# Performance work log

Measured on AMD Instinct MI355X. Metric: run time of the kernel, lower is better.

Reference implementation:

```python
import jax, jax.numpy as jnp
import numpy as np

TAU = 0.4
EPS = 1e-8


def setup_inputs() -> dict:
    key = jax.random.key(0)
    k1, k2 = jax.random.split(key)
    B, N, C, M = 4, 4096, 256, 2048
    l_feat = jax.random.normal(k1, (B, N, C), dtype=jnp.float32)
    g_feat = jax.random.normal(k2, (B, C, M), dtype=jnp.float32)
    return {"l_feat": l_feat, "g_feat": g_feat}


def reference(l_feat, g_feat):
    # l_feat: [B, N, C], g_feat: [B, C, M]
    # cosine similarity over channel dim C (torch CosineSimilarity, dim=2)
    l_norm = jnp.linalg.norm(l_feat, axis=2)          # [B, N]
    g_norm = jnp.linalg.norm(g_feat, axis=1)          # [B, M]
    dot = jnp.einsum('bnc,bcm->bnm', l_feat, g_feat)  # [B, N, M]
    cos_sim = dot / jnp.maximum(l_norm[:, :, None] * g_norm[:, None, :], EPS)
    sim = jnp.exp(cos_sim / TAU)                      # [B, N, M]
    # diag_embed(rowsum) followed by linalg.inv and bmm is exactly
    # row-wise division by the degree (row sum)
    sim = sim / jnp.sum(sim, axis=2, keepdims=True)
    # bmm(sim, g_feat^T): [B,N,M] x [B,M,C] -> [B,N,C]
    g_enh = jnp.einsum('bnm,bcm->bnc', sim, g_feat)
    return l_feat + g_enh
```

## Files before the change

### kernel.cpp

```cpp
#include <hip/hip_runtime.h>

#define B_ 4
#define N_ 4096
#define C_ 256
#define M_ 2048

typedef __attribute__((ext_vector_type(8))) short short8;
typedef __attribute__((ext_vector_type(4))) short short4v;
typedef __attribute__((ext_vector_type(4))) float f32x4;

union U16x8 { uint4 u4; unsigned short us[8]; short8 s8; };
union U16x4 { uint2 u2; unsigned short us[4]; short4v s4; };

__device__ __forceinline__ float bf2f(unsigned short h) {
    unsigned int u = ((unsigned int)h) << 16;
    return __builtin_bit_cast(float, u);
}
__device__ __forceinline__ unsigned short f2bf(float f) {
    unsigned int u = __builtin_bit_cast(unsigned int, f);
    u += 0x7FFFu + ((u >> 16) & 1u);
    return (unsigned short)(u >> 16);
}

#define GLB_AS(p) ((const __attribute__((address_space(1))) unsigned int*)(p))
#define LDS_AS(p) ((__attribute__((address_space(3))) unsigned int*)(p))

__device__ __forceinline__ f32x4 mfma16x16(short4v a, short4v b, f32x4 c) {
#if __has_builtin(__builtin_amdgcn_mfma_f32_16x16x16bf16_1k)
    return __builtin_amdgcn_mfma_f32_16x16x16bf16_1k(a, b, c, 0, 0, 0);
#else
    asm("v_mfma_f32_16x16x16_bf16 %0, %1, %2, %0" : "+v"(c) : "v"(a), "v"(b));
    return c;
#endif
}

__global__ __launch_bounds__(256) void k_norm(const float* __restrict__ g,
                                              float* __restrict__ invgn) {
    __shared__ float red[4][64];
    const int b = blockIdx.y, m0 = blockIdx.x * 64;
    const int tid = threadIdx.x;
    const int ml = tid & 63, cq = tid >> 6;
    const float* gb = g + (size_t)b * C_ * M_ + m0 + ml;
    float ss = 0.f;
#pragma unroll 8
    for (int i = 0; i < 64; ++i) {
        float v = gb[(size_t)(cq * 64 + i) * M_];
        ss += v * v;
    }
    red[cq][ml] = ss;
    __syncthreads();
    if (cq == 0) {
        float t = red[0][ml] + red[1][ml] + red[2][ml] + red[3][ml];
        invgn[b * M_ + m0 + ml] = 1.f / fmaxf(sqrtf(t), 1e-8f);
    }
}

__global__ __launch_bounds__(256) void k_cast(const float* __restrict__ g,
                                              const float* __restrict__ invgn,
                                              unsigned short* __restrict__ gcm,
                                              unsigned short* __restrict__ gmc) {
    __shared__ unsigned short T[64 * 66];
    __shared__ float sInv[64];
    const int b = blockIdx.z, c0 = blockIdx.y * 64, m0 = blockIdx.x * 64;
    const int tid = threadIdx.x;
    if (tid < 64) sInv[tid] = invgn[b * M_ + m0 + tid];
    __syncthreads();
    const float* gbase = g + ((size_t)b * C_ + c0) * M_ + m0;
    unsigned short* gcmb = gcm + ((size_t)b * C_ + c0) * M_ + m0;
#pragma unroll
    for (int j = 0; j < 4; ++j) {
        int id = tid + 256 * j;
        int ci = id >> 4, mq = (id & 15) * 4;
        float4 v = *(const float4*)(gbase + (size_t)ci * M_ + mq);
        uint2 pk;
        pk.x = (unsigned)f2bf(v.x) | ((unsigned)f2bf(v.y) << 16);
        pk.y = (unsigned)f2bf(v.z) | ((unsigned)f2bf(v.w) << 16);
        *(uint2*)(gcmb + (size_t)ci * M_ + mq) = pk;
        T[ci * 66 + mq + 0] = f2bf(v.x * sInv[mq + 0]);
        T[ci * 66 + mq + 1] = f2bf(v.y * sInv[mq + 1]);
        T[ci * 66 + mq + 2] = f2bf(v.z * sInv[mq + 2]);
        T[ci * 66 + mq + 3] = f2bf(v.w * sInv[mq + 3]);
    }
    __syncthreads();
    unsigned short* gmcb = gmc + ((size_t)b * M_ + m0) * C_ + c0;
#pragma unroll
    for (int j = 0; j < 2; ++j) {
        int id = tid + 256 * j;
        int mr = id >> 3, cc8 = (id & 7) * 8;
        U16x8 t;
#pragma unroll
        for (int k = 0; k < 8; ++k) t.us[k] = T[(cc8 + k) * 66 + mr];
        *(uint4*)(gmcb + (size_t)mr * C_ + cc8) = t.u4;
    }
}

__global__ __launch_bounds__(256, 2) void k_main(
    const float* __restrict__ l,
    const unsigned short* __restrict__ gcm,
    const unsigned short* __restrict__ gmc,
    float* __restrict__ out)
{
    __shared__ __align__(16) char sMem[66048];
    unsigned short* sGmc = (unsigned short*)sMem;
    unsigned short* sGcm = (unsigned short*)(sMem + 32768);
    float (*sDenW)[32] = (float (*)[32])(sMem + 65536);

    const int tid = threadIdx.x;
    const int w = tid >> 6;
    const int lane = tid & 63;
    const int l15 = lane & 15;
    const int quad = lane >> 4;

    const int bid = blockIdx.x;
    const int xcd = bid & 7;
    const int b = xcd >> 1;
    const int row0 = (((bid >> 3) << 1) | (xcd & 1)) * 32;

    int goffA[8], goffB[8];
#pragma unroll
    for (int i = 0; i < 8; ++i) {
        int p = (w * 8 + i) * 64 + lane;
        int rA = p >> 5;
        goffA[i] = rA * 256 + (((p & 31) ^ (rA & 31)) << 3);
        int rB = p >> 3;
        goffB[i] = rB * 2048 + (((p & 7) ^ ((rB >> 1) & 7)) << 3);
    }

    const unsigned short* gmc_b = gmc + (size_t)b * M_ * C_;
    const unsigned short* gcm_b = gcm + (size_t)b * C_ * M_;

    auto dmaA = [&](int m0) {
#pragma unroll
        for (int i = 0; i < 8; ++i)
            __builtin_amdgcn_global_load_lds(GLB_AS(gmc_b + (size_t)m0 * 256 + goffA[i]),
                                             LDS_AS(&sGmc[(w * 8 + i) * 512]), 16, 0, 0);
    };
    auto dmaB = [&](int m0) {
#pragma unroll
        for (int i = 0; i < 8; ++i)
            __builtin_amdgcn_global_load_lds(GLB_AS(gcm_b + (size_t)m0 + goffB[i]),
                                             LDS_AS(&sGcm[(w * 8 + i) * 512]), 16, 0, 0);
    };

    dmaA(0);
    dmaB(0);

    short8 qf[2][8];
#pragma unroll
    for (int rt = 0; rt < 2; ++rt) {
        const float* lrow = l + ((size_t)b * N_ + row0 + rt * 16 + l15) * C_;
        U16x8 qt[8];
        float ss = 0.f;
#pragma unroll
        for (int kk = 0; kk < 8; ++kk) {
            float4 x0 = *(const float4*)(lrow + kk * 32 + quad * 8);
            float4 x1 = *(const float4*)(lrow + kk * 32 + quad * 8 + 4);
            ss += x0.x*x0.x + x0.y*x0.y + x0.z*x0.z + x0.w*x0.w;
            ss += x1.x*x1.x + x1.y*x1.y + x1.z*x1.z + x1.w*x1.w;
            qt[kk].us[0] = f2bf(x0.x); qt[kk].us[1] = f2bf(x0.y);
            qt[kk].us[2] = f2bf(x0.z); qt[kk].us[3] = f2bf(x0.w);
            qt[kk].us[4] = f2bf(x1.x); qt[kk].us[5] = f2bf(x1.y);
            qt[kk].us[6] = f2bf(x1.z); qt[kk].us[7] = f2bf(x1.w);
        }
        ss += __shfl_xor(ss, 16);
        ss += __shfl_xor(ss, 32);
        const float invl = 1.0f / fmaxf(sqrtf(ss), 1e-8f);
#pragma unroll
        for (int kk = 0; kk < 8; ++kk) {
            U16x8 t;
#pragma unroll
            for (int j = 0; j < 8; ++j) t.us[j] = f2bf(bf2f(qt[kk].us[j]) * invl);
            qf[rt][kk] = t.s8;
        }
    }

    __syncthreads();

    f32x4 zero = {0.f, 0.f, 0.f, 0.f};
    f32x4 o[2][16];
#pragma unroll
    for (int i = 0; i < 2; ++i)
#pragma unroll
        for (int j = 0; j < 16; ++j) o[i][j] = zero;
    float dl0 = 0.f, dl1 = 0.f;

    const unsigned short* gAbase = &sGmc[(w * 16 + l15) * 256];
    const int rxor = (w * 16 + l15) & 31;
    const int chunkXor = (w * 4 + quad) ^ (l15 & 14);
    const unsigned short* gBbase = &sGcm[l15 * 64 + (chunkXor << 2)];

    for (int mt = 0; mt < 32; ++mt) {
        f32x4 sa0 = zero, sa1 = zero;
#pragma unroll
        for (int kk = 0; kk < 8; ++kk) {
            short8 ag = *(const short8*)&gAbase[((kk * 4 + quad) ^ rxor) << 3];
            sa0 = __builtin_amdgcn_mfma_f32_16x16x32_bf16(ag, qf[0][kk], sa0, 0, 0, 0);
            sa1 = __builtin_amdgcn_mfma_f32_16x16x32_bf16(ag, qf[1][kk], sa1, 0, 0, 0);
        }
        U16x4 pk0, pk1;
#pragma unroll
        for (int r = 0; r < 4; ++r) {
            float p0 = exp2f(sa0[r] * 3.6067376022224085f);
            float p1 = exp2f(sa1[r] * 3.6067376022224085f);
            dl0 += p0; dl1 += p1;
            pk0.us[r] = f2bf(p0);
            pk1.us[r] = f2bf(p1);
        }
        __syncthreads();
        if (mt < 31) dmaA((mt + 1) * 64);

#pragma unroll
        for (int ct = 0; ct < 16; ++ct) {
            short4v bb = *(const short4v*)&gBbase[ct * 1024];
            o[0][ct] = mfma16x16(pk0.s4, bb, o[0][ct]);
            o[1][ct] = mfma16x16(pk1.s4, bb, o[1][ct]);
        }
        __syncthreads();
        if (mt < 31) dmaB((mt + 1) * 64);
    }

    {
        float d0 = dl0;
        d0 += __shfl_xor(d0, 16);
        d0 += __shfl_xor(d0, 32);
        float d1 = dl1;
        d1 += __shfl_xor(d1, 16);
        d1 += __shfl_xor(d1, 32);
        if (quad == 0) {
            sDenW[w][l15] = d0;
            sDenW[w][16 + l15] = d1;
        }
    }

    f32x4* red = (f32x4*)sMem;
    const int wbase = w * 1024 + quad * 16 + l15;
    const int rbase0 = (4 * w) * 64 + quad * 16 + l15;
    f32x4 oacc0[4], oacc1[4];

    __syncthreads();
#pragma unroll
    for (int j = 0; j < 16; ++j) red[wbase + j * 64] = o[0][j];
    __syncthreads();
#pragma unroll
    for (int jj = 0; jj < 4; ++jj) {
        const int base = rbase0 + jj * 64;
        oacc0[jj] = red[base] + red[base + 1024] + red[base + 2048] + red[base + 3072];
    }
    __syncthreads();
#pragma unroll
    for (int j = 0; j < 16; ++j) red[wbase + j * 64] = o[1][j];
    __syncthreads();
#pragma unroll
    for (int jj = 0; jj < 4; ++jj) {
        const int base = rbase0 + jj * 64;
        oacc1[jj] = red[base] + red[base + 1024] + red[base + 2048] + red[base + 3072];
    }

    const float* lb = l + ((size_t)b * N_ + row0) * C_;
    float* ob = out + ((size_t)b * N_ + row0) * C_;
#pragma unroll
    for (int r = 0; r < 4; ++r) {
        {
            const int row = quad * 4 + r;
            const float inv = 1.f / (sDenW[0][row] + sDenW[1][row] + sDenW[2][row] + sDenW[3][row]);
            const size_t rb = (size_t)row * C_;
#pragma unroll
            for (int jj = 0; jj < 4; ++jj) {
                const int c = w * 64 + jj * 16 + l15;
                ob[rb + c] = lb[rb + c] + oacc0[jj][r] * inv;
            }
        }
        {
            const int row = 16 + quad * 4 + r;
            const float inv = 1.f / (sDenW[0][row] + sDenW[1][row] + sDenW[2][row] + sDenW[3][row]);
            const size_t rb = (size_t)row * C_;
#pragma unroll
            for (int jj = 0; jj < 4; ++jj) {
                const int c = w * 64 + jj * 16 + l15;
                ob[rb + c] = lb[rb + c] + oacc1[jj][r] * inv;
            }
        }
    }
}

extern "C" void kernel_launch(void* const* d_in, const int* in_sizes, int n_in,
                              void* d_out, int out_size, void* d_ws, size_t ws_size,
                              hipStream_t stream) {
    (void)in_sizes; (void)n_in; (void)out_size; (void)ws_size;
    const float* l = (const float*)d_in[0];
    const float* g = (const float*)d_in[1];
    float* outp = (float*)d_out;

    char* ws = (char*)d_ws;
    unsigned short* gmc = (unsigned short*)ws;
    unsigned short* gcm = (unsigned short*)(ws + (size_t)B_ * M_ * C_ * 2);
    float* invgn = (float*)(ws + 2 * (size_t)B_ * M_ * C_ * 2);

    k_norm<<<dim3(M_ / 64, B_), 256, 0, stream>>>(g, invgn);
    k_cast<<<dim3(M_ / 64, C_ / 64, B_), 256, 0, stream>>>(g, invgn, gcm, gmc);
    k_main<<<dim3(N_ / 32 * B_), 256, 0, stream>>>(l, gcm, gmc, outp);
}
```

Measured before the change: 144.9 us.

## Fuse norm and cast prep kernels; double rows per main block with 512 threads

The g-norm and bf16 cast/transpose kernels are merged into one prep kernel that computes the inverse norms in shared memory and then loops over channel tiles, removing one launch and the invgn round trip. The main kernel now uses 512 threads covering 64 query rows (two row-halves of 4 waves each) sharing the same staged g tiles in LDS. This halves the global/LDS traffic for g per row processed and halves the grid size. In exchange, the prep kernel has less parallelism (128 blocks looping serially over C), and the cross-wave reduction is serialized into four rounds.

```diff
diff --git a/kernel.cpp b/kernel.cpp
--- a/kernel.cpp
+++ b/kernel.cpp
@@ -34,12 +34,16 @@
 #endif
 }
 
-__global__ __launch_bounds__(256) void k_norm(const float* __restrict__ g,
-                                              float* __restrict__ invgn) {
+__global__ __launch_bounds__(256) void k_prep(const float* __restrict__ g,
+                                              unsigned short* __restrict__ gcm,
+                                              unsigned short* __restrict__ gmc) {
     __shared__ float red[4][64];
+    __shared__ float sInv[64];
+    __shared__ unsigned short T[64 * 66];
     const int b = blockIdx.y, m0 = blockIdx.x * 64;
     const int tid = threadIdx.x;
     const int ml = tid & 63, cq = tid >> 6;
+
     const float* gb = g + (size_t)b * C_ * M_ + m0 + ml;
     float ss = 0.f;
 #pragma unroll 8
@@ -51,75 +55,70 @@
     __syncthreads();
     if (cq == 0) {
         float t = red[0][ml] + red[1][ml] + red[2][ml] + red[3][ml];
-        invgn[b * M_ + m0 + ml] = 1.f / fmaxf(sqrtf(t), 1e-8f);
-    }
-}
-
-__global__ __launch_bounds__(256) void k_cast(const float* __restrict__ g,
-                                              const float* __restrict__ invgn,
-                                              unsigned short* __restrict__ gcm,
-                                              unsigned short* __restrict__ gmc) {
-    __shared__ unsigned short T[64 * 66];
-    __shared__ float sInv[64];
-    const int b = blockIdx.z, c0 = blockIdx.y * 64, m0 = blockIdx.x * 64;
-    const int tid = threadIdx.x;
-    if (tid < 64) sInv[tid] = invgn[b * M_ + m0 + tid];
+        sInv[ml] = 1.f / fmaxf(sqrtf(t), 1e-8f);
+    }
     __syncthreads();
-    const float* gbase = g + ((size_t)b * C_ + c0) * M_ + m0;
-    unsigned short* gcmb = gcm + ((size_t)b * C_ + c0) * M_ + m0;
-#pragma unroll
-    for (int j = 0; j < 4; ++j) {
-        int id = tid + 256 * j;
-        int ci = id >> 4, mq = (id & 15) * 4;
-        float4 v = *(const float4*)(gbase + (size_t)ci * M_ + mq);
-        uint2 pk;
-        pk.x = (unsigned)f2bf(v.x) | ((unsigned)f2bf(v.y) << 16);
-        pk.y = (unsigned)f2bf(v.z) | ((unsigned)f2bf(v.w) << 16);
-        *(uint2*)(gcmb + (size_t)ci * M_ + mq) = pk;
-        T[ci * 66 + mq + 0] = f2bf(v.x * sInv[mq + 0]);
-        T[ci * 66 + mq + 1] = f2bf(v.y * sInv[mq + 1]);
-        T[ci * 66 + mq + 2] = f2bf(v.z * sInv[mq + 2]);
-        T[ci * 66 + mq + 3] = f2bf(v.w * sInv[mq + 3]);
-    }
-    __syncthreads();
-    unsigned short* gmcb = gmc + ((size_t)b * M_ + m0) * C_ + c0;
-#pragma unroll
-    for (int j = 0; j < 2; ++j) {
-        int id = tid + 256 * j;
-        int mr = id >> 3, cc8 = (id & 7) * 8;
-        U16x8 t;
-#pragma unroll
-        for (int k = 0; k < 8; ++k) t.us[k] = T[(cc8 + k) * 66 + mr];
-        *(uint4*)(gmcb + (size_t)mr * C_ + cc8) = t.u4;
-    }
-}
-
-__global__ __launch_bounds__(256, 2) void k_main(
+
+    for (int c0 = 0; c0 < C_; c0 += 64) {
+        const float* gbase = g + ((size_t)b * C_ + c0) * M_ + m0;
+        unsigned short* gcmb = gcm + ((size_t)b * C_ + c0) * M_ + m0;
+#pragma unroll
+        for (int j = 0; j < 4; ++j) {
+            int id = tid + 256 * j;
+            int ci = id >> 4, mq = (id & 15) * 4;
+            float4 v = *(const float4*)(gbase + (size_t)ci * M_ + mq);
+            uint2 pk;
+            pk.x = (unsigned)f2bf(v.x) | ((unsigned)f2bf(v.y) << 16);
+            pk.y = (unsigned)f2bf(v.z) | ((unsigned)f2bf(v.w) << 16);
+            *(uint2*)(gcmb + (size_t)ci * M_ + mq) = pk;
+            T[ci * 66 + mq + 0] = f2bf(v.x * sInv[mq + 0]);
+            T[ci * 66 + mq + 1] = f2bf(v.y * sInv[mq + 1]);
+            T[ci * 66 + mq + 2] = f2bf(v.z * sInv[mq + 2]);
+            T[ci * 66 + mq + 3] = f2bf(v.w * sInv[mq + 3]);
+        }
+        __syncthreads();
+        unsigned short* gmcb = gmc + ((size_t)b * M_ + m0) * C_ + c0;
+#pragma unroll
+        for (int j = 0; j < 2; ++j) {
+            int id = tid + 256 * j;
+            int mr = id >> 3, cc8 = (id & 7) * 8;
+            U16x8 t;
+#pragma unroll
+            for (int k = 0; k < 8; ++k) t.us[k] = T[(cc8 + k) * 66 + mr];
+            *(uint4*)(gmcb + (size_t)mr * C_ + cc8) = t.u4;
+        }
+        __syncthreads();
+    }
+}
+
+__global__ __launch_bounds__(512, 2) void k_main(
     const float* __restrict__ l,
     const unsigned short* __restrict__ gcm,
     const unsigned short* __restrict__ gmc,
     float* __restrict__ out)
 {
-    __shared__ __align__(16) char sMem[66048];
+    __shared__ __align__(16) char sMem[66560];
     unsigned short* sGmc = (unsigned short*)sMem;
     unsigned short* sGcm = (unsigned short*)(sMem + 32768);
-    float (*sDenW)[32] = (float (*)[32])(sMem + 65536);
+    float (*sDen)[64] = (float (*)[64])(sMem + 65536);
 
     const int tid = threadIdx.x;
     const int w = tid >> 6;
     const int lane = tid & 63;
     const int l15 = lane & 15;
     const int quad = lane >> 4;
+    const int kh = w & 3;
+    const int rh = w >> 2;
 
     const int bid = blockIdx.x;
     const int xcd = bid & 7;
     const int b = xcd >> 1;
-    const int row0 = (((bid >> 3) << 1) | (xcd & 1)) * 32;
-
-    int goffA[8], goffB[8];
-#pragma unroll
-    for (int i = 0; i < 8; ++i) {
-        int p = (w * 8 + i) * 64 + lane;
+    const int row0 = (((bid >> 3) << 1) | (xcd & 1)) * 64;
+
+    int goffA[4], goffB[4];
+#pragma unroll
+    for (int i = 0; i < 4; ++i) {
+        int p = (w * 4 + i) * 64 + lane;
         int rA = p >> 5;
         goffA[i] = rA * 256 + (((p & 31) ^ (rA & 31)) << 3);
         int rB = p >> 3;
@@ -131,15 +130,15 @@
 
     auto dmaA = [&](int m0) {
 #pragma unroll
-        for (int i = 0; i < 8; ++i)
+        for (int i = 0; i < 4; ++i)
             __builtin_amdgcn_global_load_lds(GLB_AS(gmc_b + (size_t)m0 * 256 + goffA[i]),
-                                             LDS_AS(&sGmc[(w * 8 + i) * 512]), 16, 0, 0);
+                                             LDS_AS(&sGmc[(w * 4 + i) * 512]), 16, 0, 0);
     };
     auto dmaB = [&](int m0) {
 #pragma unroll
-        for (int i = 0; i < 8; ++i)
+        for (int i = 0; i < 4; ++i)
             __builtin_amdgcn_global_load_lds(GLB_AS(gcm_b + (size_t)m0 + goffB[i]),
-                                             LDS_AS(&sGcm[(w * 8 + i) * 512]), 16, 0, 0);
+                                             LDS_AS(&sGcm[(w * 4 + i) * 512]), 16, 0, 0);
     };
 
     dmaA(0);
@@ -148,7 +147,7 @@
     short8 qf[2][8];
 #pragma unroll
     for (int rt = 0; rt < 2; ++rt) {
-        const float* lrow = l + ((size_t)b * N_ + row0 + rt * 16 + l15) * C_;
+        const float* lrow = l + ((size_t)b * N_ + row0 + rh * 32 + rt * 16 + l15) * C_;
         U16x8 qt[8];
         float ss = 0.f;
 #pragma unroll
@@ -184,9 +183,9 @@
         for (int j = 0; j < 16; ++j) o[i][j] = zero;
     float dl0 = 0.f, dl1 = 0.f;
 
-    const unsigned short* gAbase = &sGmc[(w * 16 + l15) * 256];
-    const int rxor = (w * 16 + l15) & 31;
-    const int chunkXor = (w * 4 + quad) ^ (l15 & 14);
+    const unsigned short* gAbase = &sGmc[(kh * 16 + l15) * 256];
+    const int rxor = (kh * 16 + l15) & 31;
+    const int chunkXor = (kh * 4 + quad) ^ (l15 & 14);
     const unsigned short* gBbase = &sGcm[l15 * 64 + (chunkXor << 2)];
 
     for (int mt = 0; mt < 32; ++mt) {
@@ -227,56 +226,61 @@
         d1 += __shfl_xor(d1, 16);
         d1 += __shfl_xor(d1, 32);
         if (quad == 0) {
-            sDenW[w][l15] = d0;
-            sDenW[w][16 + l15] = d1;
-        }
-    }
-
-    f32x4* red = (f32x4*)sMem;
-    const int wbase = w * 1024 + quad * 16 + l15;
-    const int rbase0 = (4 * w) * 64 + quad * 16 + l15;
+            sDen[kh][rh * 32 + l15] = d0;
+            sDen[kh][rh * 32 + 16 + l15] = d1;
+        }
+    }
+
+    f32x4* red4 = (f32x4*)sMem;
+    const int wslot = kh * 1024 + quad * 16 + l15;
+    const int rslot = (4 * kh) * 64 + quad * 16 + l15;
     f32x4 oacc0[4], oacc1[4];
 
-    __syncthreads();
-#pragma unroll
-    for (int j = 0; j < 16; ++j) red[wbase + j * 64] = o[0][j];
-    __syncthreads();
-#pragma unroll
-    for (int jj = 0; jj < 4; ++jj) {
-        const int base = rbase0 + jj * 64;
-        oacc0[jj] = red[base] + red[base + 1024] + red[base + 2048] + red[base + 3072];
-    }
-    __syncthreads();
-#pragma unroll
-    for (int j = 0; j < 16; ++j) red[wbase + j * 64] = o[1][j];
-    __syncthreads();
-#pragma unroll
-    for (int jj = 0; jj < 4; ++jj) {
-        const int base = rbase0 + jj * 64;
-        oacc1[jj] = red[base] + red[base + 1024] + red[base + 2048] + red[base + 3072];
-    }
-
-    const float* lb = l + ((size_t)b * N_ + row0) * C_;
-    float* ob = out + ((size_t)b * N_ + row0) * C_;
+#define RED_ROUND(RH, OSRC, ODST)                                              \
+    __syncthreads();                                                           \
+    if (rh == (RH)) {                                                          \
+        _Pragma("unroll")                                                      \
+        for (int j = 0; j < 16; ++j) red4[wslot + j * 64] = OSRC[j];           \
+    }                                                                          \
+    __syncthreads();                                                           \
+    if (rh == (RH)) {                                                          \
+        _Pragma("unroll")                                                      \
+        for (int jj = 0; jj < 4; ++jj) {                                       \
+            const int base = rslot + jj * 64;                                  \
+            ODST[jj] = red4[base] + red4[base + 1024] +                        \
+                       red4[base + 2048] + red4[base + 3072];                  \
+        }                                                                      \
+    }
+
+    RED_ROUND(0, o[0], oacc0)
+    RED_ROUND(0, o[1], oacc1)
+    RED_ROUND(1, o[0], oacc0)
+    RED_ROUND(1, o[1], oacc1)
+#undef RED_ROUND
+
+    const float* lb = l + ((size_t)b * N_ + row0 + rh * 32) * C_;
+    float* ob = out + ((size_t)b * N_ + row0 + rh * 32) * C_;
 #pragma unroll
     for (int r = 0; r < 4; ++r) {
         {
             const int row = quad * 4 + r;
-            const float inv = 1.f / (sDenW[0][row] + sDenW[1][row] + sDenW[2][row] + sDenW[3][row]);
+            const int grow = rh * 32 + row;
+            const float inv = 1.f / (sDen[0][grow] + sDen[1][grow] + sDen[2][grow] + sDen[3][grow]);
             const size_t rb = (size_t)row * C_;
 #pragma unroll
             for (int jj = 0; jj < 4; ++jj) {
-                const int c = w * 64 + jj * 16 + l15;
+                const int c = kh * 64 + jj * 16 + l15;
                 ob[rb + c] = lb[rb + c] + oacc0[jj][r] * inv;
             }
         }
         {
             const int row = 16 + quad * 4 + r;
-            const float inv = 1.f / (sDenW[0][row] + sDenW[1][row] + sDenW[2][row] + sDenW[3][row]);
+            const int grow = rh * 32 + row;
+            const float inv = 1.f / (sDen[0][grow] + sDen[1][grow] + sDen[2][grow] + sDen[3][grow]);
             const size_t rb = (size_t)row * C_;
 #pragma unroll
             for (int jj = 0; jj < 4; ++jj) {
-                const int c = w * 64 + jj * 16 + l15;
+                const int c = kh * 64 + jj * 16 + l15;
                 ob[rb + c] = lb[rb + c] + oacc1[jj][r] * inv;
             }
         }
@@ -294,9 +298,7 @@
     char* ws = (char*)d_ws;
     unsigned short* gmc = (unsigned short*)ws;
     unsigned short* gcm = (unsigned short*)(ws + (size_t)B_ * M_ * C_ * 2);
-    float* invgn = (float*)(ws + 2 * (size_t)B_ * M_ * C_ * 2);
-
-    k_norm<<<dim3(M_ / 64, B_), 256, 0, stream>>>(g, invgn);
-    k_cast<<<dim3(M_ / 64, C_ / 64, B_), 256, 0, stream>>>(g, invgn, gcm, gmc);
-    k_main<<<dim3(N_ / 32 * B_), 256, 0, stream>>>(l, gcm, gmc, outp);
-}
+
+    k_prep<<<dim3(M_ / 64, B_), 256, 0, stream>>>(g, gcm, gmc);
+    k_main<<<dim3(N_ / 64 * B_), 512, 0, stream>>>(l, gcm, gmc, outp);
+}
```

Result: faster. 139.7 us (-3.6%).
